# Kernel optimization log

Hardware: AMD Instinct MI355X
Metric: run time of the kernel (lower is better)

The kernel has to match this reference:

```python
import jax, jax.numpy as jnp
import numpy as np

B, C, L = 64, 128, 1024
SCALES = [8, 4, 2, 1]
EPS_BN = 1e-5


def _ema_vec(x_ds, alpha):
    # x_ds: [B, C, Ls]; alpha: [1, C, 1] in (0,1)
    Ls = x_ds.shape[-1]
    powers = jnp.arange(Ls - 1, -1, -1, dtype=x_ds.dtype)
    base = jnp.power(1.0 - alpha, powers)                                 # [1, C, Ls]
    w_num = jnp.concatenate([base[..., :1], base[..., 1:] * alpha], axis=-1)
    num = jnp.cumsum(x_ds * w_num, axis=-1)
    den = jnp.maximum(jnp.cumsum(base, axis=-1), 1e-12)
    return num / den


def _dwconv(x, w, s):
    # depthwise Conv1d: kernel 2s, stride s, pad s//2, groups=C, no bias
    return jax.lax.conv_general_dilated(
        x, w, window_strides=(s,), padding=[(s // 2, s // 2)],
        dimension_numbers=("NCH", "OIH", "NCH"), feature_group_count=C)


def _proj(v, w1, b1, w2, b2):
    # v: [B, C, Ls] -> Linear(Ls->L), exact GELU, Linear(L->L); torch Linear y = x @ W.T + b
    h = jax.nn.gelu(jnp.einsum("bcs,ls->bcl", v, w1) + b1, approximate=False)
    return jnp.einsum("bcl,ml->bcm", h, w2) + b2


def _hasd(x, bn_g, bn_b, branch, gate):
    Bn = x.shape[0]
    # BatchNorm1d over flattened (C*L) features, training-mode batch stats (biased var)
    v = x.reshape(Bn, C * L)
    mu = v.mean(axis=0)
    var = jnp.mean((v - mu) ** 2, axis=0)
    xn = (((v - mu) / jnp.sqrt(var + EPS_BN)) * bn_g + bn_b).reshape(Bn, C, L)
    trends, seasons, gates = [], [], []
    for s in SCALES:
        if s > 1:
            cw, w1, b1, w2, b2 = branch[s]
            down = _dwconv(xn, cw, s)                                     # [B, C, L//s]
            up = _proj(down, w1, b1, w2, b2)                              # [B, C, L]
        else:
            down = xn
            up = xn
        gw, gb, al = gate[s]
        alpha = jax.nn.sigmoid(al)
        trend_ds = _ema_vec(down, alpha)
        trend_up = _proj(trend_ds, w1, b1, w2, b2) if s > 1 else trend_ds
        season = up - trend_up
        trends.append(trend_up)
        seasons.append(season)
        gates.append(jax.nn.sigmoid(season.mean(axis=-1) @ gw.T + gb))    # [B, 1]
    g = jnp.concatenate(gates, axis=1)                                    # [B, n_scales]
    g = g / (g.sum(axis=1, keepdims=True) + 1e-6)
    g = g[:, :, None, None]
    trend_out = (jnp.stack(trends, axis=1) * g).sum(axis=1)
    season_out = (jnp.stack(seasons, axis=1) * g).sum(axis=1)
    return season_out, trend_out


def setup_inputs() -> dict:
    key = jax.random.key(0)
    ks = iter(jax.random.split(key, 64))
    d = {"x": jax.random.normal(next(ks), (B, C, L), jnp.float32)}
    d["bn_g"] = 1.0 + 0.1 * jax.random.normal(next(ks), (C * L,), jnp.float32)
    d["bn_b"] = 0.1 * jax.random.normal(next(ks), (C * L,), jnp.float32)
    for s in (8, 4, 2):
        Ls = L // s
        d[f"cw{s}"] = jax.random.normal(next(ks), (C, 1, 2 * s), jnp.float32) / np.sqrt(2 * s)
        d[f"w1_{s}"] = jax.random.normal(next(ks), (L, Ls), jnp.float32) / np.sqrt(Ls)
        d[f"b1_{s}"] = jnp.zeros((L,), jnp.float32)
        d[f"w2_{s}"] = jax.random.normal(next(ks), (L, L), jnp.float32) / np.sqrt(L)
        d[f"b2_{s}"] = jnp.zeros((L,), jnp.float32)
    for s in SCALES:
        d[f"gw{s}"] = jax.random.normal(next(ks), (1, C), jnp.float32) / np.sqrt(C)
        d[f"gb{s}"] = jnp.zeros((1,), jnp.float32)
        d[f"al{s}"] = jnp.full((1, C, 1), 0.3, jnp.float32)
    return d


def reference(x, bn_g, bn_b,
              cw8, w1_8, b1_8, w2_8, b2_8,
              cw4, w1_4, b1_4, w2_4, b2_4,
              cw2, w1_2, b1_2, w2_2, b2_2,
              gw8, gb8, al8, gw4, gb4, al4, gw2, gb2, al2, gw1, gb1, al1):
    branch = {8: (cw8, w1_8, b1_8, w2_8, b2_8),
              4: (cw4, w1_4, b1_4, w2_4, b2_4),
              2: (cw2, w1_2, b1_2, w2_2, b2_2)}
    gate = {8: (gw8, gb8, al8), 4: (gw4, gb4, al4),
            2: (gw2, gb2, al2), 1: (gw1, gb1, al1)}
    return _hasd(x, bn_g, bn_b, branch, gate)
```

## Files before the change

### kernel.cpp

```cpp
#include <hip/hip_runtime.h>
#include <hip/hip_bf16.h>
#include <math.h>

#define Bdim 64
#define Cdim 128
#define Ldim 1024
#define BC   (Bdim * Cdim)
#define CLn  (Cdim * Ldim)
#define TOT  (Bdim * CLn)

typedef unsigned short ushort_t;
typedef short s16x8 __attribute__((ext_vector_type(8)));
typedef float f32x4 __attribute__((ext_vector_type(4)));

__device__ __forceinline__ float bf2f(ushort_t u) {
    return __uint_as_float(((unsigned)u) << 16);
}
__device__ __forceinline__ ushort_t f2bf(float f) {
    __hip_bfloat16 h = __float2bfloat16(f);
    return *(ushort_t*)&h;
}
__device__ __forceinline__ void async16(const ushort_t* g, ushort_t* l) {
    __builtin_amdgcn_global_load_lds(
        (const __attribute__((address_space(1))) unsigned int*)g,
        (__attribute__((address_space(3))) unsigned int*)l, 16, 0, 0);
}
__device__ __forceinline__ float fast_gelu(float z) {
    float z2 = z * z;
    float inner = fmaf(0.044715f * z2, z, z);
    float e = __expf(-1.5957691216057308f * inner);
    return z * __builtin_amdgcn_rcpf(1.f + e);
}

__global__ __launch_bounds__(256) void bn_stats_kernel(
    const float* __restrict__ x, const float* __restrict__ bn_g,
    const float* __restrict__ bn_b, float* __restrict__ scale,
    float* __restrict__ shift)
{
    int f = blockIdx.x * 256 + threadIdx.x;
    float sum = 0.f, sumsq = 0.f;
    for (int b = 0; b < Bdim; ++b) {
        float v = x[(size_t)b * CLn + f];
        sum += v; sumsq += v * v;
    }
    float mu  = sum * (1.f / Bdim);
    float var = fmaxf(sumsq * (1.f / Bdim) - mu * mu, 0.f);
    float sc  = bn_g[f] / sqrtf(var + 1e-5f);
    scale[f] = sc;
    shift[f] = bn_b[f] - mu * sc;
}

__global__ __launch_bounds__(256) void convert_weights_kernel(
    const float* __restrict__ w1_8, const float* __restrict__ w1_4,
    const float* __restrict__ w1_2, const float* __restrict__ w2_8,
    const float* __restrict__ w2_4, const float* __restrict__ w2_2,
    ushort_t* __restrict__ dst)
{
    int idx = blockIdx.x * 256 + threadIdx.x;
    const float* src; int off;
    if      (idx < 131072)  { src = w1_8; off = 0; }
    else if (idx < 393216)  { src = w1_4; off = 131072; }
    else if (idx < 917504)  { src = w1_2; off = 393216; }
    else if (idx < 1966080) { src = w2_8; off = 917504; }
    else if (idx < 3014656) { src = w2_4; off = 1966080; }
    else                    { src = w2_2; off = 3014656; }
    dst[idx] = f2bf(src[idx - off]);
}

__global__ __launch_bounds__(256) void w2colsum_kernel(
    const float* __restrict__ w2_8, const float* __restrict__ w2_4,
    const float* __restrict__ w2_2, float* __restrict__ w2cs)
{
    const float* w = (blockIdx.y == 0) ? w2_8 : (blockIdx.y == 1) ? w2_4 : w2_2;
    int h  = blockIdx.x * 64 + (threadIdx.x & 63);
    int ls = threadIdx.x >> 6;
    float s = 0.f;
    for (int l = ls; l < 1024; l += 4) s += w[(size_t)l * 1024 + h];
    __shared__ float red[4][64];
    red[ls][threadIdx.x & 63] = s;
    __syncthreads();
    if (ls == 0)
        w2cs[blockIdx.y * 1024 + h] =
            red[0][threadIdx.x] + red[1][threadIdx.x] +
            red[2][threadIdx.x] + red[3][threadIdx.x];
}

__global__ __launch_bounds__(256) void ema_coef_kernel(
    const float* __restrict__ al1, const float* __restrict__ al2,
    const float* __restrict__ al4, const float* __restrict__ al8,
    float* __restrict__ coef, float* __restrict__ am)
{
    int c   = blockIdx.x;
    int tid = threadIdx.x;
    const float* als[4] = {al1, al2, al4, al8};
    const int Lss[4]    = {1024, 512, 256, 128};
    const int offs[4]   = {0, 1024, 1536, 1792};
#pragma unroll
    for (int si = 0; si < 4; ++si) {
        double a  = 1.0 / (1.0 + exp(-(double)als[si][c]));
        double m  = 1.0 - a;
        double lm = log(m);
        int Ls = Lss[si];
        for (int t = tid; t < Ls; t += 256) {
            double dt  = (1.0 - exp((double)(t + 1) * lm)) / a;
            double den = exp((double)(Ls - 1 - t) * lm) * dt;
            double ramp = (den >= 1e-12) ? 1.0 : den * 1e12;
            coef[(size_t)c * 1920 + offs[si] + t] = (float)(ramp / dt);
        }
        if (tid == 0) {
            am[c * 8 + si * 2 + 0] = (float)a;
            am[c * 8 + si * 2 + 1] = (float)m;
        }
    }
}

template<int SEG>
__device__ __forceinline__ void ema_pass1(
    const float* __restrict__ src, float a, float m, bool lead,
    float* __restrict__ xs, float& Sp, float& Sm)
{
    int lane = threadIdx.x & 63;
    if constexpr (SEG >= 4) {
#pragma unroll
        for (int i = 0; i < SEG; i += 4) {
            f32x4 u = *(const f32x4*)&src[lane * SEG + i];
            xs[i + 0] = u.x; xs[i + 1] = u.y;
            xs[i + 2] = u.z; xs[i + 3] = u.w;
        }
    } else {
        float2 u = *(const float2*)&src[lane * 2];
        xs[0] = u.x; xs[1] = u.y;
    }
    float p = 0.f;
#pragma unroll
    for (int i = 0; i < SEG; ++i) {
        float bi = a * xs[i];
        if (lead && lane == 0 && i == 0) bi = xs[0];
        p = fmaf(m, p, bi);
    }
    float sm = m;
#pragma unroll
    for (int i = 1; i < SEG; ++i) sm *= m;
    Sp = p; Sm = sm;
#pragma unroll
    for (int d = 1; d < 64; d <<= 1) {
        float pm = __shfl_up(Sp, d);
        float mm = __shfl_up(Sm, d);
        if (lane >= d) { Sp = fmaf(Sm, pm, Sp); Sm *= mm; }
    }
}

template<int SEG, bool DIFF>
__device__ __forceinline__ float ema_pass2(
    const float* __restrict__ xs, float a, float m, bool lead, float carry,
    const float* __restrict__ cf, ushort_t* __restrict__ dst)
{
    int lane = threadIdx.x & 63;
    float y = carry, diff = 0.f;
    unsigned pk[(SEG + 1) / 2];
#pragma unroll
    for (int i = 0; i < SEG; ++i) {
        float bi = a * xs[i];
        if (lead && lane == 0 && i == 0) bi = xs[0];
        y = fmaf(m, y, bi);
        float tr = y * cf[lane * SEG + i];
        unsigned h = f2bf(tr);
        if ((i & 1) == 0) pk[i >> 1] = h;
        else              pk[i >> 1] |= h << 16;
        if (DIFF) diff += xs[i] - tr;
    }
    if constexpr (SEG == 8) {
        uint4 v; v.x = pk[0]; v.y = pk[1]; v.z = pk[2]; v.w = pk[3];
        *(uint4*)(dst + lane * 8) = v;
    } else if constexpr (SEG == 4) {
        uint2 v; v.x = pk[0]; v.y = pk[1];
        *(uint2*)(dst + lane * 4) = v;
    } else {
        *(unsigned*)(dst + lane * 2) = pk[0];
    }
    return diff;
}

__global__ __launch_bounds__(256) void pre_kernel(
    const float* __restrict__ x, const float* __restrict__ scale,
    const float* __restrict__ shift,
    const float* __restrict__ cw8, const float* __restrict__ cw4,
    const float* __restrict__ cw2,
    const float* __restrict__ coef, const float* __restrict__ amtab,
    ushort_t* __restrict__ xn_bf, ushort_t* __restrict__ t1_bf,
    ushort_t* __restrict__ A8, ushort_t* __restrict__ A4,
    ushort_t* __restrict__ A2, float* __restrict__ rs)
{
    __shared__ float sxn[1024];
    __shared__ float sxnp[1056];
    __shared__ float sconv[896];
    __shared__ float sP0;
    __shared__ float sdiff[2];
    int r   = blockIdx.x;
    int c   = r & (Cdim - 1);
    int tid = threadIdx.x;

    {
        const float* xr = x + (size_t)r * 1024;
        float4 xv = *(const float4*)(xr + tid * 4);
        float4 sc = *(const float4*)(scale + (size_t)c * 1024 + tid * 4);
        float4 sh = *(const float4*)(shift + (size_t)c * 1024 + tid * 4);
        float v0 = fmaf(xv.x, sc.x, sh.x);
        float v1 = fmaf(xv.y, sc.y, sh.y);
        float v2 = fmaf(xv.z, sc.z, sh.z);
        float v3 = fmaf(xv.w, sc.w, sh.w);
        int p = tid * 4;
        sxn[p + 0] = v0; sxn[p + 1] = v1; sxn[p + 2] = v2; sxn[p + 3] = v3;
        int pp = p + (p >> 5);
        sxnp[pp + 0] = v0; sxnp[pp + 1] = v1;
        sxnp[pp + 2] = v2; sxnp[pp + 3] = v3;
        uint2 pk;
        pk.x = (unsigned)f2bf(v0) | ((unsigned)f2bf(v1) << 16);
        pk.y = (unsigned)f2bf(v2) | ((unsigned)f2bf(v3) << 16);
        *(uint2*)(xn_bf + (size_t)r * 1024 + tid * 4) = pk;
    }
    __syncthreads();

    {
        const float* w2 = cw2 + c * 4;
        unsigned a2pk = 0;
#pragma unroll
        for (int j = 0; j < 2; ++j) {
            int o = tid * 2 + j;
            int start = o * 2 - 1;
            float acc = 0.f;
#pragma unroll
            for (int k = 0; k < 4; ++k) {
                int pos = start + k;
                float v = (pos >= 0 && pos < 1024) ? sxnp[pos + (pos >> 5)] : 0.f;
                acc = fmaf(v, w2[k], acc);
            }
            sconv[o] = acc;
            a2pk |= ((unsigned)f2bf(acc)) << (j * 16);
        }
        *(unsigned*)(A2 + (size_t)r * 512 + tid * 2) = a2pk;
        {
            const float* w4 = cw4 + c * 8;
            int o = tid;
            int start = o * 4 - 2;
            float acc = 0.f;
#pragma unroll
            for (int k = 0; k < 8; ++k) {
                int pos = start + k;
                float v = (pos >= 0 && pos < 1024) ? sxnp[pos + (pos >> 5)] : 0.f;
                acc = fmaf(v, w4[k], acc);
            }
            sconv[512 + o] = acc;
            A4[(size_t)r * 256 + o] = f2bf(acc);
        }
        if (tid < 128) {
            const float* w8 = cw8 + c * 16;
            int o = tid;
            int start = o * 8 - 4;
            float acc = 0.f;
#pragma unroll
            for (int k = 0; k < 16; ++k) {
                int pos = start + k;
                float v = (pos >= 0 && pos < 1024) ? sxnp[pos + (pos >> 5)] : 0.f;
                acc = fmaf(v, w8[k], acc);
            }
            sconv[768 + o] = acc;
            A8[(size_t)r * 128 + o] = f2bf(acc);
        }
    }
    __syncthreads();

    int wave = tid >> 6;
    int lane = tid & 63;
    const float* cf = coef + (size_t)c * 1920;
    const float* am = amtab + c * 8;
    float xs[8];
    float Sp = 0.f, Sm = 1.f, aE = 0.f, mE = 0.f;

    if (wave == 0) {
        aE = am[0]; mE = am[1];
        ema_pass1<8>(sxn, aE, mE, true, xs, Sp, Sm);
        if (lane == 63) sP0 = Sp;
    } else if (wave == 1) {
        aE = am[0]; mE = am[1];
        ema_pass1<8>(sxn + 512, aE, mE, false, xs, Sp, Sm);
    } else if (wave == 2) {
        aE = am[2]; mE = am[3];
        ema_pass1<8>(sconv, aE, mE, true, xs, Sp, Sm);
    } else {
        aE = am[4]; mE = am[5];
        ema_pass1<4>(sconv + 512, aE, mE, true, xs, Sp, Sm);
    }
    __syncthreads();

    float cs  = __shfl_up(Sp, 1);
    float msf = __shfl_up(Sm, 1);
    float carry = lane ? cs : 0.f;

    if (wave == 0) {
        float d = ema_pass2<8, true>(xs, aE, mE, true, carry,
                                     cf, t1_bf + (size_t)r * 1024);
#pragma unroll
        for (int dd = 32; dd; dd >>= 1) d += __shfl_down(d, dd);
        if (lane == 0) sdiff[0] = d;
    } else if (wave == 1) {
        carry += sP0 * (lane ? msf : 1.f);
        float d = ema_pass2<8, true>(xs, aE, mE, false, carry,
                                     cf + 512, t1_bf + (size_t)r * 1024 + 512);
#pragma unroll
        for (int dd = 32; dd; dd >>= 1) d += __shfl_down(d, dd);
        if (lane == 0) sdiff[1] = d;
    } else if (wave == 2) {
        ema_pass2<8, false>(xs, aE, mE, true, carry,
                            cf + 1024, A2 + ((size_t)BC + r) * 512);
    } else {
        ema_pass2<4, false>(xs, aE, mE, true, carry,
                            cf + 1536, A4 + ((size_t)BC + r) * 256);
        float xs2[2];
        aE = am[6]; mE = am[7];
        ema_pass1<2>(sconv + 768, aE, mE, true, xs2, Sp, Sm);
        float cs2 = __shfl_up(Sp, 1);
        float c2  = lane ? cs2 : 0.f;
        ema_pass2<2, false>(xs2, aE, mE, true, c2,
                            cf + 1792, A8 + ((size_t)BC + r) * 128);
    }
    __syncthreads();
    if (tid == 0) rs[3 * BC + r] = sdiff[0] + sdiff[1];
}

__global__ __launch_bounds__(256) void gemm1_kernel(
    const ushort_t* __restrict__ Abase,
    const ushort_t* __restrict__ Wbase,
    const float* __restrict__ b1_8, const float* __restrict__ b1_4,
    const float* __restrict__ b1_2, const float* __restrict__ w2cs,
    ushort_t* __restrict__ Hbase, float* __restrict__ rs)
{
    int z = blockIdx.z;
    int K = 128 << z;
    const ushort_t* A  = Abase + (size_t)2 * BC * 128 * ((1 << z) - 1);
    const ushort_t* Bw = Wbase + (size_t)131072 * ((1 << z) - 1);
    const float* bias  = (z == 0) ? b1_8 : (z == 1) ? b1_4 : b1_2;
    ushort_t* Hout     = Hbase + (size_t)z * 2 * TOT;

    __shared__ ushort_t As[128 * 64];
    __shared__ ushort_t Bs[128 * 64];
    int tid  = threadIdx.x;
    int wave = tid >> 6;
    int lane = tid & 63;
    int m0 = blockIdx.x * 128, n0 = blockIdx.y * 128;
    int wm = (wave & 1) * 64, wn = (wave >> 1) * 64;
    int lrow = lane >> 3;
    int pc   = lane & 7;
    int fr   = lane & 15;
    int quad = lane >> 4;

    f32x4 acc[4][4];
#pragma unroll
    for (int i = 0; i < 4; ++i)
#pragma unroll
        for (int j = 0; j < 4; ++j) acc[i][j] = (f32x4){0.f, 0.f, 0.f, 0.f};

    for (int k0 = 0; k0 < K; k0 += 64) {
        __syncthreads();
#pragma unroll
        for (int i = 0; i < 4; ++i) {
            int rb  = wave * 32 + i * 8;
            int row = rb + lrow;
            int lc  = (pc - row) & 7;
            async16(A  + (size_t)(m0 + row) * K + k0 + lc * 8, &As[rb * 64]);
            async16(Bw + (size_t)(n0 + row) * K + k0 + lc * 8, &Bs[rb * 64]);
        }
        __syncthreads();
#pragma unroll
        for (int kk = 0; kk < 64; kk += 32) {
            s16x8 af[4], bfr[4];
            int lcA = (kk >> 3) + quad;
#pragma unroll
            for (int t = 0; t < 4; ++t) {
                int mr  = wm + t * 16 + fr;
                af[t]  = *(const s16x8*)&As[mr * 64 + ((lcA + mr) & 7) * 8];
                int nr  = wn + t * 16 + fr;
                bfr[t] = *(const s16x8*)&Bs[nr * 64 + ((lcA + nr) & 7) * 8];
            }
#pragma unroll
            for (int mt = 0; mt < 4; ++mt)
#pragma unroll
                for (int nt = 0; nt < 4; ++nt)
                    acc[mt][nt] = __builtin_amdgcn_mfma_f32_16x16x32_bf16(
                        af[mt], bfr[nt], acc[mt][nt], 0, 0, 0);
        }
    }
    int is_trend = (m0 >= BC);
    float sign = is_trend ? -1.f : 1.f;
    float racc[16];
#pragma unroll
    for (int e = 0; e < 16; ++e) racc[e] = 0.f;
#pragma unroll
    for (int mt = 0; mt < 4; ++mt)
#pragma unroll
        for (int nt = 0; nt < 4; ++nt) {
            int col = n0 + wn + nt * 16 + fr;
            float wcs = w2cs[z * 1024 + col];
#pragma unroll
            for (int rr = 0; rr < 4; ++rr) {
                size_t row = m0 + wm + mt * 16 + quad * 4 + rr;
                float zv = acc[mt][nt][rr] + bias[col];
                float zg = fast_gelu(zv);
                Hout[row * 1024 + col] = f2bf(zg);
                racc[mt * 4 + rr] = fmaf(zg, wcs, racc[mt * 4 + rr]);
            }
        }
#pragma unroll
    for (int e = 0; e < 16; ++e) {
        float v = racc[e];
        v += __shfl_xor(v, 1); v += __shfl_xor(v, 2);
        v += __shfl_xor(v, 4); v += __shfl_xor(v, 8);
        if (fr == 0) {
            int mt = e >> 2, rr = e & 3;
            int row = m0 + wm + mt * 16 + quad * 4 + rr;
            int ra  = row - (is_trend ? BC : 0);
            atomicAdd(&rs[z * BC + ra], sign * v);
        }
    }
}

template<int IS_U>
__global__ __launch_bounds__(256) void gemm2_kernel(
    const ushort_t* __restrict__ Hbase,
    const ushort_t* __restrict__ W2base,
    const float* __restrict__ b2_8, const float* __restrict__ b2_4,
    const float* __restrict__ b2_2, const float* __restrict__ g,
    const ushort_t* __restrict__ aux,
    const float* __restrict__ trend_in,
    float* __restrict__ outp)
{
    __shared__ ushort_t As[128 * 64];
    __shared__ ushort_t Bs[128 * 64];
    int tid  = threadIdx.x;
    int wave = tid >> 6;
    int lane = tid & 63;
    int m0 = blockIdx.x * 128, n0 = blockIdx.y * 128;
    int wm = (wave & 1) * 64, wn = (wave >> 1) * 64;
    int lrow = lane >> 3;
    int pc   = lane & 7;
    int fr   = lane & 15;
    int quad = lane >> 4;
    int b = m0 >> 7;
    float gv0 = g[b * 4 + 0], gv1 = g[b * 4 + 1], gv2 = g[b * 4 + 2];
    float g1  = g[b * 4 + 3];
    float gsv[3] = {gv0, gv1, gv2};

    f32x4 acc[4][4];
#pragma unroll
    for (int i = 0; i < 4; ++i)
#pragma unroll
        for (int j = 0; j < 4; ++j) acc[i][j] = (f32x4){0.f, 0.f, 0.f, 0.f};

    for (int s = 0; s < 3; ++s) {
        if (s > 0) {
            float rr_ = gsv[s - 1] / fmaxf(gsv[s], 1e-30f);
#pragma unroll
            for (int mt = 0; mt < 4; ++mt)
#pragma unroll
                for (int nt = 0; nt < 4; ++nt)
#pragma unroll
                    for (int rr = 0; rr < 4; ++rr)
                        acc[mt][nt][rr] *= rr_;
        }
        const ushort_t* A  = Hbase + (size_t)s * 2 * TOT + (IS_U ? 0 : TOT);
        const ushort_t* Bw = W2base + (size_t)s * 1048576;
        for (int k0 = 0; k0 < 1024; k0 += 64) {
            __syncthreads();
#pragma unroll
            for (int i = 0; i < 4; ++i) {
                int rb  = wave * 32 + i * 8;
                int row = rb + lrow;
                int lc  = (pc - row) & 7;
                async16(A  + (size_t)(m0 + row) * 1024 + k0 + lc * 8, &As[rb * 64]);
                async16(Bw + (size_t)(n0 + row) * 1024 + k0 + lc * 8, &Bs[rb * 64]);
            }
            __syncthreads();
#pragma unroll
            for (int kk = 0; kk < 64; kk += 32) {
                s16x8 af[4], bfr[4];
                int lcA = (kk >> 3) + quad;
#pragma unroll
                for (int t = 0; t < 4; ++t) {
                    int mr  = wm + t * 16 + fr;
                    af[t]  = *(const s16x8*)&As[mr * 64 + ((lcA + mr) & 7) * 8];
                    int nr  = wn + t * 16 + fr;
                    bfr[t] = *(const s16x8*)&Bs[nr * 64 + ((lcA + nr) & 7) * 8];
                }
#pragma unroll
                for (int mt = 0; mt < 4; ++mt)
#pragma unroll
                    for (int nt = 0; nt < 4; ++nt)
                        acc[mt][nt] = __builtin_amdgcn_mfma_f32_16x16x32_bf16(
                            af[mt], bfr[nt], acc[mt][nt], 0, 0, 0);
            }
        }
    }
#pragma unroll
    for (int mt = 0; mt < 4; ++mt)
#pragma unroll
        for (int nt = 0; nt < 4; ++nt)
#pragma unroll
            for (int rr = 0; rr < 4; ++rr)
                acc[mt][nt][rr] *= gv2;

#pragma unroll
    for (int mt = 0; mt < 4; ++mt)
#pragma unroll
        for (int nt = 0; nt < 4; ++nt) {
            int col = n0 + wn + nt * 16 + fr;
            float cb2 = gv0 * b2_8[col] + gv1 * b2_4[col] + gv2 * b2_2[col];
#pragma unroll
            for (int r = 0; r < 4; ++r) {
                size_t row = m0 + wm + mt * 16 + quad * 4 + r;
                size_t idx = row * 1024 + col;
                float v = acc[mt][nt][r] + cb2 + g1 * bf2f(aux[idx]);
                if (IS_U) v -= trend_in[idx];
                outp[idx] = v;
            }
        }
}

__global__ __launch_bounds__(128) void gate_kernel(
    const float* __restrict__ rs,
    const float* __restrict__ gw8, const float* __restrict__ gb8,
    const float* __restrict__ gw4, const float* __restrict__ gb4,
    const float* __restrict__ gw2, const float* __restrict__ gb2,
    const float* __restrict__ gw1, const float* __restrict__ gb1,
    float* __restrict__ g)
{
    int b = blockIdx.x;
    int c = threadIdx.x;
    const float* gws[4] = {gw8, gw4, gw2, gw1};
    const float* gbs[4] = {gb8, gb4, gb2, gb1};
    __shared__ float buf[128];
    __shared__ float gates[4];
    for (int si = 0; si < 4; ++si) {
        buf[c] = rs[si * BC + b * Cdim + c] * (1.f / Ldim) * gws[si][c];
        __syncthreads();
        for (int off = 64; off >= 1; off >>= 1) {
            if (c < off) buf[c] += buf[c + off];
            __syncthreads();
        }
        if (c == 0) {
            float z = buf[0] + gbs[si][0];
            gates[si] = 1.f / (1.f + expf(-z));
        }
        __syncthreads();
    }
    if (c == 0) {
        float s = gates[0] + gates[1] + gates[2] + gates[3] + 1e-6f;
#pragma unroll
        for (int si = 0; si < 4; ++si) g[b * 4 + si] = gates[si] / s;
    }
}

extern "C" void kernel_launch(void* const* d_in, const int* in_sizes, int n_in,
                              void* d_out, int out_size, void* d_ws, size_t ws_size,
                              hipStream_t stream)
{
    const float* x    = (const float*)d_in[0];
    const float* bn_g = (const float*)d_in[1];
    const float* bn_b = (const float*)d_in[2];
    const float* cw8  = (const float*)d_in[3];
    const float* w1_8 = (const float*)d_in[4];
    const float* b1_8 = (const float*)d_in[5];
    const float* w2_8 = (const float*)d_in[6];
    const float* b2_8 = (const float*)d_in[7];
    const float* cw4  = (const float*)d_in[8];
    const float* w1_4 = (const float*)d_in[9];
    const float* b1_4 = (const float*)d_in[10];
    const float* w2_4 = (const float*)d_in[11];
    const float* b2_4 = (const float*)d_in[12];
    const float* cw2  = (const float*)d_in[13];
    const float* w1_2 = (const float*)d_in[14];
    const float* b1_2 = (const float*)d_in[15];
    const float* w2_2 = (const float*)d_in[16];
    const float* b2_2 = (const float*)d_in[17];
    const float* gw8  = (const float*)d_in[18];
    const float* gb8  = (const float*)d_in[19];
    const float* al8  = (const float*)d_in[20];
    const float* gw4  = (const float*)d_in[21];
    const float* gb4  = (const float*)d_in[22];
    const float* al4  = (const float*)d_in[23];
    const float* gw2  = (const float*)d_in[24];
    const float* gb2  = (const float*)d_in[25];
    const float* al2  = (const float*)d_in[26];
    const float* gw1  = (const float*)d_in[27];
    const float* gb1  = (const float*)d_in[28];
    const float* al1  = (const float*)d_in[29];

    ushort_t* p_xn  = (ushort_t*)d_ws;
    ushort_t* p_t1  = p_xn + TOT;
    ushort_t* p_H   = p_t1 + TOT;
    ushort_t* p_wb  = p_H + 6 * (size_t)TOT;
    ushort_t* p_w1b = p_wb;
    ushort_t* p_w2b = p_wb + 917504;
    float*    p_sc  = (float*)(p_wb + 4063232);
    float*    p_sh  = p_sc + CLn;
    float*    p_w2cs = p_sh + CLn;
    float*    p_rs  = p_w2cs + 3 * 1024;
    float*    p_g   = p_rs + 4 * BC;
    float*    p_coef = (float*)p_H;
    float*    p_am   = p_coef + 128 * 1920;
    ushort_t* p_A8 = (ushort_t*)d_out;
    ushort_t* p_A4 = p_A8 + 2 * (size_t)BC * 128;
    ushort_t* p_A2 = p_A4 + 2 * (size_t)BC * 256;
    float*    p_season = (float*)d_out;
    float*    p_trend  = (float*)d_out + TOT;

    hipMemsetAsync(p_rs, 0, 4 * BC * sizeof(float), stream);
    bn_stats_kernel<<<CLn / 256, 256, 0, stream>>>(x, bn_g, bn_b, p_sc, p_sh);
    ema_coef_kernel<<<128, 256, 0, stream>>>(al1, al2, al4, al8, p_coef, p_am);
    convert_weights_kernel<<<4063232 / 256, 256, 0, stream>>>(
        w1_8, w1_4, w1_2, w2_8, w2_4, w2_2, p_wb);
    w2colsum_kernel<<<dim3(16, 3), 256, 0, stream>>>(w2_8, w2_4, w2_2, p_w2cs);

    pre_kernel<<<BC, 256, 0, stream>>>(x, p_sc, p_sh, cw8, cw4, cw2,
                                       p_coef, p_am,
                                       p_xn, p_t1, p_A8, p_A4, p_A2, p_rs);

    gemm1_kernel<<<dim3(128, 8, 3), 256, 0, stream>>>(
        p_A8, p_w1b, b1_8, b1_4, b1_2, p_w2cs, p_H, p_rs);

    gate_kernel<<<Bdim, 128, 0, stream>>>(p_rs, gw8, gb8, gw4, gb4,
                                          gw2, gb2, gw1, gb1, p_g);

    dim3 g2(64, 8);
    gemm2_kernel<0><<<g2, 256, 0, stream>>>(p_H, p_w2b, b2_8, b2_4, b2_2,
                                            p_g, p_t1, nullptr, p_trend);
    gemm2_kernel<1><<<g2, 256, 0, stream>>>(p_H, p_w2b, b2_8, b2_4, b2_2,
                                            p_g, p_xn, p_trend, p_season);
}
```

Before: 458.3 us.

## Share W tiles between up and trend rows in both GEMMs

```diff
diff --git a/kernel.cpp b/kernel.cpp
--- a/kernel.cpp
+++ b/kernel.cpp
@@ -328,37 +328,43 @@
     if (tid == 0) rs[3 * BC + r] = sdiff[0] + sdiff[1];
 }
 
-__global__ __launch_bounds__(256) void gemm1_kernel(
+__global__ __launch_bounds__(256, 2) void gemm1_kernel(
     const ushort_t* __restrict__ Abase,
     const ushort_t* __restrict__ Wbase,
     const float* __restrict__ b1_8, const float* __restrict__ b1_4,
     const float* __restrict__ b1_2, const float* __restrict__ w2cs,
     ushort_t* __restrict__ Hbase, float* __restrict__ rs)
 {
-    int z = blockIdx.z;
+    int gx = blockIdx.x;
+    int z  = 2 - (gx >> 6);
+    int mi = gx & 63;
     int K = 128 << z;
     const ushort_t* A  = Abase + (size_t)2 * BC * 128 * ((1 << z) - 1);
     const ushort_t* Bw = Wbase + (size_t)131072 * ((1 << z) - 1);
     const float* bias  = (z == 0) ? b1_8 : (z == 1) ? b1_4 : b1_2;
     ushort_t* Hout     = Hbase + (size_t)z * 2 * TOT;
 
-    __shared__ ushort_t As[128 * 64];
+    __shared__ ushort_t Asu[128 * 64];
+    __shared__ ushort_t Ast[128 * 64];
     __shared__ ushort_t Bs[128 * 64];
     int tid  = threadIdx.x;
     int wave = tid >> 6;
     int lane = tid & 63;
-    int m0 = blockIdx.x * 128, n0 = blockIdx.y * 128;
+    int m0 = mi * 128, n0 = blockIdx.y * 128;
     int wm = (wave & 1) * 64, wn = (wave >> 1) * 64;
     int lrow = lane >> 3;
     int pc   = lane & 7;
     int fr   = lane & 15;
     int quad = lane >> 4;
 
-    f32x4 acc[4][4];
+    f32x4 accu[4][4], acct[4][4];
 #pragma unroll
     for (int i = 0; i < 4; ++i)
 #pragma unroll
-        for (int j = 0; j < 4; ++j) acc[i][j] = (f32x4){0.f, 0.f, 0.f, 0.f};
+        for (int j = 0; j < 4; ++j) {
+            accu[i][j] = (f32x4){0.f, 0.f, 0.f, 0.f};
+            acct[i][j] = (f32x4){0.f, 0.f, 0.f, 0.f};
+        }
 
     for (int k0 = 0; k0 < K; k0 += 64) {
         __syncthreads();
@@ -367,8 +373,9 @@
             int rb  = wave * 32 + i * 8;
             int row = rb + lrow;
             int lc  = (pc - row) & 7;
-            async16(A  + (size_t)(m0 + row) * K + k0 + lc * 8, &As[rb * 64]);
-            async16(Bw + (size_t)(n0 + row) * K + k0 + lc * 8, &Bs[rb * 64]);
+            async16(A + (size_t)(m0 + row) * K + k0 + lc * 8,      &Asu[rb * 64]);
+            async16(A + (size_t)(BC + m0 + row) * K + k0 + lc * 8, &Ast[rb * 64]);
+            async16(Bw + (size_t)(n0 + row) * K + k0 + lc * 8,     &Bs[rb * 64]);
         }
         __syncthreads();
 #pragma unroll
@@ -377,21 +384,33 @@
             int lcA = (kk >> 3) + quad;
 #pragma unroll
             for (int t = 0; t < 4; ++t) {
-                int mr  = wm + t * 16 + fr;
-                af[t]  = *(const s16x8*)&As[mr * 64 + ((lcA + mr) & 7) * 8];
                 int nr  = wn + t * 16 + fr;
                 bfr[t] = *(const s16x8*)&Bs[nr * 64 + ((lcA + nr) & 7) * 8];
             }
 #pragma unroll
+            for (int t = 0; t < 4; ++t) {
+                int mr  = wm + t * 16 + fr;
+                af[t]  = *(const s16x8*)&Asu[mr * 64 + ((lcA + mr) & 7) * 8];
+            }
+#pragma unroll
             for (int mt = 0; mt < 4; ++mt)
 #pragma unroll
                 for (int nt = 0; nt < 4; ++nt)
-                    acc[mt][nt] = __builtin_amdgcn_mfma_f32_16x16x32_bf16(
-                        af[mt], bfr[nt], acc[mt][nt], 0, 0, 0);
-        }
-    }
-    int is_trend = (m0 >= BC);
-    float sign = is_trend ? -1.f : 1.f;
+                    accu[mt][nt] = __builtin_amdgcn_mfma_f32_16x16x32_bf16(
+                        af[mt], bfr[nt], accu[mt][nt], 0, 0, 0);
+#pragma unroll
+            for (int t = 0; t < 4; ++t) {
+                int mr  = wm + t * 16 + fr;
+                af[t]  = *(const s16x8*)&Ast[mr * 64 + ((lcA + mr) & 7) * 8];
+            }
+#pragma unroll
+            for (int mt = 0; mt < 4; ++mt)
+#pragma unroll
+                for (int nt = 0; nt < 4; ++nt)
+                    acct[mt][nt] = __builtin_amdgcn_mfma_f32_16x16x32_bf16(
+                        af[mt], bfr[nt], acct[mt][nt], 0, 0, 0);
+        }
+    }
     float racc[16];
 #pragma unroll
     for (int e = 0; e < 16; ++e) racc[e] = 0.f;
@@ -400,14 +419,16 @@
 #pragma unroll
         for (int nt = 0; nt < 4; ++nt) {
             int col = n0 + wn + nt * 16 + fr;
+            float bcol = bias[col];
             float wcs = w2cs[z * 1024 + col];
 #pragma unroll
             for (int rr = 0; rr < 4; ++rr) {
                 size_t row = m0 + wm + mt * 16 + quad * 4 + rr;
-                float zv = acc[mt][nt][rr] + bias[col];
-                float zg = fast_gelu(zv);
-                Hout[row * 1024 + col] = f2bf(zg);
-                racc[mt * 4 + rr] = fmaf(zg, wcs, racc[mt * 4 + rr]);
+                float gu = fast_gelu(accu[mt][nt][rr] + bcol);
+                float gt = fast_gelu(acct[mt][nt][rr] + bcol);
+                Hout[row * 1024 + col]        = f2bf(gu);
+                Hout[(BC + row) * 1024 + col] = f2bf(gt);
+                racc[mt * 4 + rr] = fmaf(gu - gt, wcs, racc[mt * 4 + rr]);
             }
         }
 #pragma unroll
@@ -418,23 +439,21 @@
         if (fr == 0) {
             int mt = e >> 2, rr = e & 3;
             int row = m0 + wm + mt * 16 + quad * 4 + rr;
-            int ra  = row - (is_trend ? BC : 0);
-            atomicAdd(&rs[z * BC + ra], sign * v);
-        }
-    }
-}
-
-template<int IS_U>
-__global__ __launch_bounds__(256) void gemm2_kernel(
+            atomicAdd(&rs[z * BC + row], v);
+        }
+    }
+}
+
+__global__ __launch_bounds__(256, 2) void gemm2_kernel(
     const ushort_t* __restrict__ Hbase,
     const ushort_t* __restrict__ W2base,
     const float* __restrict__ b2_8, const float* __restrict__ b2_4,
     const float* __restrict__ b2_2, const float* __restrict__ g,
-    const ushort_t* __restrict__ aux,
-    const float* __restrict__ trend_in,
-    float* __restrict__ outp)
-{
-    __shared__ ushort_t As[128 * 64];
+    const ushort_t* __restrict__ t1_bf, const ushort_t* __restrict__ xn_bf,
+    float* __restrict__ trend_out, float* __restrict__ season_out)
+{
+    __shared__ ushort_t Asu[128 * 64];
+    __shared__ ushort_t Ast[128 * 64];
     __shared__ ushort_t Bs[128 * 64];
     int tid  = threadIdx.x;
     int wave = tid >> 6;
@@ -450,11 +469,14 @@
     float g1  = g[b * 4 + 3];
     float gsv[3] = {gv0, gv1, gv2};
 
-    f32x4 acc[4][4];
+    f32x4 accu[4][4], acct[4][4];
 #pragma unroll
     for (int i = 0; i < 4; ++i)
 #pragma unroll
-        for (int j = 0; j < 4; ++j) acc[i][j] = (f32x4){0.f, 0.f, 0.f, 0.f};
+        for (int j = 0; j < 4; ++j) {
+            accu[i][j] = (f32x4){0.f, 0.f, 0.f, 0.f};
+            acct[i][j] = (f32x4){0.f, 0.f, 0.f, 0.f};
+        }
 
     for (int s = 0; s < 3; ++s) {
         if (s > 0) {
@@ -464,10 +486,13 @@
 #pragma unroll
                 for (int nt = 0; nt < 4; ++nt)
 #pragma unroll
-                    for (int rr = 0; rr < 4; ++rr)
-                        acc[mt][nt][rr] *= rr_;
-        }
-        const ushort_t* A  = Hbase + (size_t)s * 2 * TOT + (IS_U ? 0 : TOT);
+                    for (int rr = 0; rr < 4; ++rr) {
+                        accu[mt][nt][rr] *= rr_;
+                        acct[mt][nt][rr] *= rr_;
+                    }
+        }
+        const ushort_t* Au = Hbase + (size_t)s * 2 * TOT;
+        const ushort_t* At = Au + TOT;
         const ushort_t* Bw = W2base + (size_t)s * 1048576;
         for (int k0 = 0; k0 < 1024; k0 += 64) {
             __syncthreads();
@@ -476,7 +501,8 @@
                 int rb  = wave * 32 + i * 8;
                 int row = rb + lrow;
                 int lc  = (pc - row) & 7;
-                async16(A  + (size_t)(m0 + row) * 1024 + k0 + lc * 8, &As[rb * 64]);
+                async16(Au + (size_t)(m0 + row) * 1024 + k0 + lc * 8, &Asu[rb * 64]);
+                async16(At + (size_t)(m0 + row) * 1024 + k0 + lc * 8, &Ast[rb * 64]);
                 async16(Bw + (size_t)(n0 + row) * 1024 + k0 + lc * 8, &Bs[rb * 64]);
             }
             __syncthreads();
@@ -486,17 +512,31 @@
                 int lcA = (kk >> 3) + quad;
 #pragma unroll
                 for (int t = 0; t < 4; ++t) {
-                    int mr  = wm + t * 16 + fr;
-                    af[t]  = *(const s16x8*)&As[mr * 64 + ((lcA + mr) & 7) * 8];
                     int nr  = wn + t * 16 + fr;
                     bfr[t] = *(const s16x8*)&Bs[nr * 64 + ((lcA + nr) & 7) * 8];
                 }
 #pragma unroll
+                for (int t = 0; t < 4; ++t) {
+                    int mr  = wm + t * 16 + fr;
+                    af[t]  = *(const s16x8*)&Asu[mr * 64 + ((lcA + mr) & 7) * 8];
+                }
+#pragma unroll
                 for (int mt = 0; mt < 4; ++mt)
 #pragma unroll
                     for (int nt = 0; nt < 4; ++nt)
-                        acc[mt][nt] = __builtin_amdgcn_mfma_f32_16x16x32_bf16(
-                            af[mt], bfr[nt], acc[mt][nt], 0, 0, 0);
+                        accu[mt][nt] = __builtin_amdgcn_mfma_f32_16x16x32_bf16(
+                            af[mt], bfr[nt], accu[mt][nt], 0, 0, 0);
+#pragma unroll
+                for (int t = 0; t < 4; ++t) {
+                    int mr  = wm + t * 16 + fr;
+                    af[t]  = *(const s16x8*)&Ast[mr * 64 + ((lcA + mr) & 7) * 8];
+                }
+#pragma unroll
+                for (int mt = 0; mt < 4; ++mt)
+#pragma unroll
+                    for (int nt = 0; nt < 4; ++nt)
+                        acct[mt][nt] = __builtin_amdgcn_mfma_f32_16x16x32_bf16(
+                            af[mt], bfr[nt], acct[mt][nt], 0, 0, 0);
             }
         }
     }
@@ -505,8 +545,10 @@
 #pragma unroll
         for (int nt = 0; nt < 4; ++nt)
 #pragma unroll
-            for (int rr = 0; rr < 4; ++rr)
-                acc[mt][nt][rr] *= gv2;
+            for (int rr = 0; rr < 4; ++rr) {
+                accu[mt][nt][rr] *= gv2;
+                acct[mt][nt][rr] *= gv2;
+            }
 
 #pragma unroll
     for (int mt = 0; mt < 4; ++mt)
@@ -518,9 +560,10 @@
             for (int r = 0; r < 4; ++r) {
                 size_t row = m0 + wm + mt * 16 + quad * 4 + r;
                 size_t idx = row * 1024 + col;
-                float v = acc[mt][nt][r] + cb2 + g1 * bf2f(aux[idx]);
-                if (IS_U) v -= trend_in[idx];
-                outp[idx] = v;
+                float tr = acct[mt][nt][r] + cb2 + g1 * bf2f(t1_bf[idx]);
+                float se = accu[mt][nt][r] + cb2 + g1 * bf2f(xn_bf[idx]) - tr;
+                trend_out[idx]  = tr;
+                season_out[idx] = se;
             }
         }
 }
@@ -624,15 +667,12 @@
                                        p_coef, p_am,
                                        p_xn, p_t1, p_A8, p_A4, p_A2, p_rs);
 
-    gemm1_kernel<<<dim3(128, 8, 3), 256, 0, stream>>>(
+    gemm1_kernel<<<dim3(192, 8), 256, 0, stream>>>(
         p_A8, p_w1b, b1_8, b1_4, b1_2, p_w2cs, p_H, p_rs);
 
     gate_kernel<<<Bdim, 128, 0, stream>>>(p_rs, gw8, gb8, gw4, gb4,
                                           gw2, gb2, gw1, gb1, p_g);
 
-    dim3 g2(64, 8);
-    gemm2_kernel<0><<<g2, 256, 0, stream>>>(p_H, p_w2b, b2_8, b2_4, b2_2,
-                                            p_g, p_t1, nullptr, p_trend);
-    gemm2_kernel<1><<<g2, 256, 0, stream>>>(p_H, p_w2b, b2_8, b2_4, b2_2,
-                                            p_g, p_xn, p_trend, p_season);
-}
+    gemm2_kernel<<<dim3(64, 8), 256, 0, stream>>>(
+        p_H, p_w2b, b2_8, b2_4, b2_2, p_g, p_t1, p_xn, p_trend, p_season);
+}
```

New measurement: 426.1 us. -7.0%, faster.

## Share weight tiles across trend/up halves and double-buffer GEMM LDS loads

Applied to the files above, without the earlier changes.

```diff
diff --git a/kernel.cpp b/kernel.cpp
--- a/kernel.cpp
+++ b/kernel.cpp
@@ -328,27 +328,31 @@
     if (tid == 0) rs[3 * BC + r] = sdiff[0] + sdiff[1];
 }
 
-__global__ __launch_bounds__(256) void gemm1_kernel(
+__global__ __launch_bounds__(512, 2) void gemm1_kernel(
     const ushort_t* __restrict__ Abase,
     const ushort_t* __restrict__ Wbase,
     const float* __restrict__ b1_8, const float* __restrict__ b1_4,
     const float* __restrict__ b1_2, const float* __restrict__ w2cs,
     ushort_t* __restrict__ Hbase, float* __restrict__ rs)
 {
-    int z = blockIdx.z;
-    int K = 128 << z;
+    __shared__ ushort_t smem[49152];
+    int gx = blockIdx.x;
+    int z  = 2 - (gx >> 6);
+    int mi = gx & 63;
+    int K  = 128 << z;
+    int NT = K >> 6;
     const ushort_t* A  = Abase + (size_t)2 * BC * 128 * ((1 << z) - 1);
     const ushort_t* Bw = Wbase + (size_t)131072 * ((1 << z) - 1);
     const float* bias  = (z == 0) ? b1_8 : (z == 1) ? b1_4 : b1_2;
     ushort_t* Hout     = Hbase + (size_t)z * 2 * TOT;
 
-    __shared__ ushort_t As[128 * 64];
-    __shared__ ushort_t Bs[128 * 64];
     int tid  = threadIdx.x;
     int wave = tid >> 6;
     int lane = tid & 63;
-    int m0 = blockIdx.x * 128, n0 = blockIdx.y * 128;
-    int wm = (wave & 1) * 64, wn = (wave >> 1) * 64;
+    int m0 = mi * 128, n0 = blockIdx.y * 128;
+    int half = wave >> 2;
+    int ws   = wave & 3;
+    int wm = (ws & 1) * 64, wn = (ws >> 1) * 64;
     int lrow = lane >> 3;
     int pc   = lane & 7;
     int fr   = lane & 15;
@@ -360,27 +364,37 @@
 #pragma unroll
         for (int j = 0; j < 4; ++j) acc[i][j] = (f32x4){0.f, 0.f, 0.f, 0.f};
 
-    for (int k0 = 0; k0 < K; k0 += 64) {
-        __syncthreads();
-#pragma unroll
-        for (int i = 0; i < 4; ++i) {
-            int rb  = wave * 32 + i * 8;
+    auto stage = [&](int t, int buf) {
+        int k0 = t * 64;
+        ushort_t* base = smem + buf * 24576;
+#pragma unroll
+        for (int i = 0; i < 2; ++i) {
+            int rb  = wave * 16 + i * 8;
             int row = rb + lrow;
             int lc  = (pc - row) & 7;
-            async16(A  + (size_t)(m0 + row) * K + k0 + lc * 8, &As[rb * 64]);
-            async16(Bw + (size_t)(n0 + row) * K + k0 + lc * 8, &Bs[rb * 64]);
-        }
-        __syncthreads();
+            async16(A  + (size_t)(m0 + row) * K + k0 + lc * 8,      base + rb * 64);
+            async16(A  + (size_t)(BC + m0 + row) * K + k0 + lc * 8, base + 8192 + rb * 64);
+            async16(Bw + (size_t)(n0 + row) * K + k0 + lc * 8,      base + 16384 + rb * 64);
+        }
+    };
+
+    stage(0, 0);
+    __syncthreads();
+    int cur = 0;
+    for (int t = 0; t < NT; ++t) {
+        if (t + 1 < NT) stage(t + 1, cur ^ 1);
+        const ushort_t* As_ = smem + cur * 24576 + half * 8192;
+        const ushort_t* Bs_ = smem + cur * 24576 + 16384;
 #pragma unroll
         for (int kk = 0; kk < 64; kk += 32) {
             s16x8 af[4], bfr[4];
             int lcA = (kk >> 3) + quad;
 #pragma unroll
-            for (int t = 0; t < 4; ++t) {
-                int mr  = wm + t * 16 + fr;
-                af[t]  = *(const s16x8*)&As[mr * 64 + ((lcA + mr) & 7) * 8];
-                int nr  = wn + t * 16 + fr;
-                bfr[t] = *(const s16x8*)&Bs[nr * 64 + ((lcA + nr) & 7) * 8];
+            for (int q = 0; q < 4; ++q) {
+                int nr  = wn + q * 16 + fr;
+                bfr[q] = *(const s16x8*)&Bs_[nr * 64 + ((lcA + nr) & 7) * 8];
+                int mr  = wm + q * 16 + fr;
+                af[q]  = *(const s16x8*)&As_[mr * 64 + ((lcA + mr) & 7) * 8];
             }
 #pragma unroll
             for (int mt = 0; mt < 4; ++mt)
@@ -389,9 +403,12 @@
                     acc[mt][nt] = __builtin_amdgcn_mfma_f32_16x16x32_bf16(
                         af[mt], bfr[nt], acc[mt][nt], 0, 0, 0);
         }
-    }
-    int is_trend = (m0 >= BC);
-    float sign = is_trend ? -1.f : 1.f;
+        __syncthreads();
+        cur ^= 1;
+    }
+
+    float sign = half ? -1.f : 1.f;
+    ushort_t* Hh = Hout + (size_t)half * BC * 1024;
     float racc[16];
 #pragma unroll
     for (int e = 0; e < 16; ++e) racc[e] = 0.f;
@@ -400,14 +417,14 @@
 #pragma unroll
         for (int nt = 0; nt < 4; ++nt) {
             int col = n0 + wn + nt * 16 + fr;
+            float bcol = bias[col];
             float wcs = w2cs[z * 1024 + col];
 #pragma unroll
             for (int rr = 0; rr < 4; ++rr) {
                 size_t row = m0 + wm + mt * 16 + quad * 4 + rr;
-                float zv = acc[mt][nt][rr] + bias[col];
-                float zg = fast_gelu(zv);
-                Hout[row * 1024 + col] = f2bf(zg);
-                racc[mt * 4 + rr] = fmaf(zg, wcs, racc[mt * 4 + rr]);
+                float gu = fast_gelu(acc[mt][nt][rr] + bcol);
+                Hh[row * 1024 + col] = f2bf(gu);
+                racc[mt * 4 + rr] = fmaf(gu, wcs, racc[mt * 4 + rr]);
             }
         }
 #pragma unroll
@@ -418,29 +435,27 @@
         if (fr == 0) {
             int mt = e >> 2, rr = e & 3;
             int row = m0 + wm + mt * 16 + quad * 4 + rr;
-            int ra  = row - (is_trend ? BC : 0);
-            atomicAdd(&rs[z * BC + ra], sign * v);
-        }
-    }
-}
-
-template<int IS_U>
-__global__ __launch_bounds__(256) void gemm2_kernel(
+            atomicAdd(&rs[z * BC + row], sign * v);
+        }
+    }
+}
+
+__global__ __launch_bounds__(512, 2) void gemm2_kernel(
     const ushort_t* __restrict__ Hbase,
     const ushort_t* __restrict__ W2base,
     const float* __restrict__ b2_8, const float* __restrict__ b2_4,
     const float* __restrict__ b2_2, const float* __restrict__ g,
-    const ushort_t* __restrict__ aux,
-    const float* __restrict__ trend_in,
-    float* __restrict__ outp)
-{
-    __shared__ ushort_t As[128 * 64];
-    __shared__ ushort_t Bs[128 * 64];
+    const ushort_t* __restrict__ t1_bf, const ushort_t* __restrict__ xn_bf,
+    float* __restrict__ trend_out, float* __restrict__ season_out)
+{
+    __shared__ ushort_t smem[49152];
     int tid  = threadIdx.x;
     int wave = tid >> 6;
     int lane = tid & 63;
     int m0 = blockIdx.x * 128, n0 = blockIdx.y * 128;
-    int wm = (wave & 1) * 64, wn = (wave >> 1) * 64;
+    int half = wave >> 2;
+    int ws   = wave & 3;
+    int wm = (ws & 1) * 64, wn = (ws >> 1) * 64;
     int lrow = lane >> 3;
     int pc   = lane & 7;
     int fr   = lane & 15;
@@ -456,8 +471,33 @@
 #pragma unroll
         for (int j = 0; j < 4; ++j) acc[i][j] = (f32x4){0.f, 0.f, 0.f, 0.f};
 
-    for (int s = 0; s < 3; ++s) {
-        if (s > 0) {
+    auto stage = [&](int kt, int buf) {
+        int s  = kt >> 4;
+        int k0 = (kt & 15) * 64;
+        const ushort_t* Au = Hbase + (size_t)s * 2 * TOT;
+        const ushort_t* At = Au + TOT;
+        const ushort_t* Bw = W2base + (size_t)s * 1048576;
+        ushort_t* base = smem + buf * 24576;
+#pragma unroll
+        for (int i = 0; i < 2; ++i) {
+            int rb  = wave * 16 + i * 8;
+            int row = rb + lrow;
+            int lc  = (pc - row) & 7;
+            size_t goff = (size_t)(m0 + row) * 1024 + k0 + lc * 8;
+            async16(Au + goff, base + rb * 64);
+            async16(At + goff, base + 8192 + rb * 64);
+            async16(Bw + (size_t)(n0 + row) * 1024 + k0 + lc * 8,
+                    base + 16384 + rb * 64);
+        }
+    };
+
+    stage(0, 0);
+    __syncthreads();
+    int cur = 0;
+    for (int kt = 0; kt < 48; ++kt) {
+        if (kt + 1 < 48) stage(kt + 1, cur ^ 1);
+        if (kt > 0 && (kt & 15) == 0) {
+            int s = kt >> 4;
             float rr_ = gsv[s - 1] / fmaxf(gsv[s], 1e-30f);
 #pragma unroll
             for (int mt = 0; mt < 4; ++mt)
@@ -467,38 +507,28 @@
                     for (int rr = 0; rr < 4; ++rr)
                         acc[mt][nt][rr] *= rr_;
         }
-        const ushort_t* A  = Hbase + (size_t)s * 2 * TOT + (IS_U ? 0 : TOT);
-        const ushort_t* Bw = W2base + (size_t)s * 1048576;
-        for (int k0 = 0; k0 < 1024; k0 += 64) {
-            __syncthreads();
-#pragma unroll
-            for (int i = 0; i < 4; ++i) {
-                int rb  = wave * 32 + i * 8;
-                int row = rb + lrow;
-                int lc  = (pc - row) & 7;
-                async16(A  + (size_t)(m0 + row) * 1024 + k0 + lc * 8, &As[rb * 64]);
-                async16(Bw + (size_t)(n0 + row) * 1024 + k0 + lc * 8, &Bs[rb * 64]);
-            }
-            __syncthreads();
-#pragma unroll
-            for (int kk = 0; kk < 64; kk += 32) {
-                s16x8 af[4], bfr[4];
-                int lcA = (kk >> 3) + quad;
-#pragma unroll
-                for (int t = 0; t < 4; ++t) {
-                    int mr  = wm + t * 16 + fr;
-                    af[t]  = *(const s16x8*)&As[mr * 64 + ((lcA + mr) & 7) * 8];
-                    int nr  = wn + t * 16 + fr;
-                    bfr[t] = *(const s16x8*)&Bs[nr * 64 + ((lcA + nr) & 7) * 8];
-                }
-#pragma unroll
-                for (int mt = 0; mt < 4; ++mt)
-#pragma unroll
-                    for (int nt = 0; nt < 4; ++nt)
-                        acc[mt][nt] = __builtin_amdgcn_mfma_f32_16x16x32_bf16(
-                            af[mt], bfr[nt], acc[mt][nt], 0, 0, 0);
-            }
-        }
+        const ushort_t* As_ = smem + cur * 24576 + half * 8192;
+        const ushort_t* Bs_ = smem + cur * 24576 + 16384;
+#pragma unroll
+        for (int kk = 0; kk < 64; kk += 32) {
+            s16x8 af[4], bfr[4];
+            int lcA = (kk >> 3) + quad;
+#pragma unroll
+            for (int q = 0; q < 4; ++q) {
+                int nr  = wn + q * 16 + fr;
+                bfr[q] = *(const s16x8*)&Bs_[nr * 64 + ((lcA + nr) & 7) * 8];
+                int mr  = wm + q * 16 + fr;
+                af[q]  = *(const s16x8*)&As_[mr * 64 + ((lcA + mr) & 7) * 8];
+            }
+#pragma unroll
+            for (int mt = 0; mt < 4; ++mt)
+#pragma unroll
+                for (int nt = 0; nt < 4; ++nt)
+                    acc[mt][nt] = __builtin_amdgcn_mfma_f32_16x16x32_bf16(
+                        af[mt], bfr[nt], acc[mt][nt], 0, 0, 0);
+        }
+        __syncthreads();
+        cur ^= 1;
     }
 #pragma unroll
     for (int mt = 0; mt < 4; ++mt)
@@ -508,21 +538,44 @@
             for (int rr = 0; rr < 4; ++rr)
                 acc[mt][nt][rr] *= gv2;
 
-#pragma unroll
-    for (int mt = 0; mt < 4; ++mt)
-#pragma unroll
-        for (int nt = 0; nt < 4; ++nt) {
-            int col = n0 + wn + nt * 16 + fr;
-            float cb2 = gv0 * b2_8[col] + gv1 * b2_4[col] + gv2 * b2_2[col];
-#pragma unroll
-            for (int r = 0; r < 4; ++r) {
-                size_t row = m0 + wm + mt * 16 + quad * 4 + r;
-                size_t idx = row * 1024 + col;
-                float v = acc[mt][nt][r] + cb2 + g1 * bf2f(aux[idx]);
-                if (IS_U) v -= trend_in[idx];
-                outp[idx] = v;
-            }
-        }
+    float* exch = (float*)smem;
+    if (half == 1) {
+#pragma unroll
+        for (int mt = 0; mt < 4; ++mt)
+#pragma unroll
+            for (int nt = 0; nt < 4; ++nt) {
+                int col = n0 + wn + nt * 16 + fr;
+                float cb2 = gv0 * b2_8[col] + gv1 * b2_4[col] + gv2 * b2_2[col];
+#pragma unroll
+                for (int rr = 0; rr < 4; ++rr) {
+                    int lm = wm + mt * 16 + quad * 4 + rr;
+                    size_t row = m0 + lm;
+                    size_t idx = row * 1024 + col;
+                    float tr = acc[mt][nt][rr] + cb2 + g1 * bf2f(t1_bf[idx]);
+                    trend_out[idx] = tr;
+                    exch[lm * 132 + wn + nt * 16 + fr] = tr;
+                }
+            }
+    }
+    __syncthreads();
+    if (half == 0) {
+#pragma unroll
+        for (int mt = 0; mt < 4; ++mt)
+#pragma unroll
+            for (int nt = 0; nt < 4; ++nt) {
+                int col = n0 + wn + nt * 16 + fr;
+                float cb2 = gv0 * b2_8[col] + gv1 * b2_4[col] + gv2 * b2_2[col];
+#pragma unroll
+                for (int rr = 0; rr < 4; ++rr) {
+                    int lm = wm + mt * 16 + quad * 4 + rr;
+                    size_t row = m0 + lm;
+                    size_t idx = row * 1024 + col;
+                    float tr = exch[lm * 132 + wn + nt * 16 + fr];
+                    float se = acc[mt][nt][rr] + cb2 + g1 * bf2f(xn_bf[idx]) - tr;
+                    season_out[idx] = se;
+                }
+            }
+    }
 }
 
 __global__ __launch_bounds__(128) void gate_kernel(
@@ -624,15 +677,12 @@
                                        p_coef, p_am,
                                        p_xn, p_t1, p_A8, p_A4, p_A2, p_rs);
 
-    gemm1_kernel<<<dim3(128, 8, 3), 256, 0, stream>>>(
+    gemm1_kernel<<<dim3(192, 8), 512, 0, stream>>>(
         p_A8, p_w1b, b1_8, b1_4, b1_2, p_w2cs, p_H, p_rs);
 
     gate_kernel<<<Bdim, 128, 0, stream>>>(p_rs, gw8, gb8, gw4, gb4,
                                           gw2, gb2, gw1, gb1, p_g);
 
-    dim3 g2(64, 8);
-    gemm2_kernel<0><<<g2, 256, 0, stream>>>(p_H, p_w2b, b2_8, b2_4, b2_2,
-                                            p_g, p_t1, nullptr, p_trend);
-    gemm2_kernel<1><<<g2, 256, 0, stream>>>(p_H, p_w2b, b2_8, b2_4, b2_2,
-                                            p_g, p_xn, p_trend, p_season);
-}
+    gemm2_kernel<<<dim3(64, 8), 512, 0, stream>>>(
+        p_H, p_w2b, b2_8, b2_4, b2_2, p_g, p_t1, p_xn, p_trend, p_season);
+}
```

Measured after the change: 441.3 us. 3.7% less time.
